# Performance work log

Hardware: AMD Instinct MI355X
Metric: run time of the kernel (lower is better)

## Reference

```python
import jax, jax.numpy as jnp
import numpy as np

B, S, H, L, NL = 64, 512, 768, 8, 10  # batch, seq, hidden, seps-per-sample ('longest'), num_labels

def setup_inputs() -> dict:
    key = jax.random.key(0)
    ks = jax.random.split(key, 16)
    sc = 0.05
    inp = {
        'electra_output': jax.random.normal(ks[0], (B, S, H), jnp.float32),
        # [SEP] locations: exactly L per sample -> mode count == L
        'sep_bx': jnp.repeat(jnp.arange(B, dtype=jnp.int64), L),
        'sep_by': jax.random.randint(ks[1], (B * L,), 1, S, dtype=jnp.int64),
        'w_ih_f': jax.random.normal(ks[2], (4 * H, H), jnp.float32) * sc,
        'w_hh_f': jax.random.normal(ks[3], (4 * H, H), jnp.float32) * sc,
        'b_ih_f': jax.random.normal(ks[4], (4 * H,), jnp.float32) * sc,
        'b_hh_f': jax.random.normal(ks[5], (4 * H,), jnp.float32) * sc,
        'w_ih_b': jax.random.normal(ks[6], (4 * H, H), jnp.float32) * sc,
        'w_hh_b': jax.random.normal(ks[7], (4 * H, H), jnp.float32) * sc,
        'b_ih_b': jax.random.normal(ks[8], (4 * H,), jnp.float32) * sc,
        'b_hh_b': jax.random.normal(ks[9], (4 * H,), jnp.float32) * sc,
        'fc1_w': jax.random.normal(ks[10], (NL, 5 * H), jnp.float32) * sc,
        'fc1_b': jax.random.normal(ks[11], (NL,), jnp.float32) * sc,
        'fc2_w': jax.random.normal(ks[12], (NL, 2 * H), jnp.float32) * sc,
        'fc2_b': jax.random.normal(ks[13], (NL,), jnp.float32) * sc,
    }
    return inp

def _lstm_dir(x, w_ih, w_hh, b_ih, b_hh):
    # x: [B, T, H] -> hs: [B, T, H]. PyTorch gate order: i, f, g, o.
    b, t, h = x.shape
    xg = jnp.einsum('bth,gh->btg', x, w_ih) + b_ih + b_hh  # [B,T,4H]
    def step(carry, xt):
        hprev, cprev = carry
        g = xt + hprev @ w_hh.T
        i, f, gg, o = jnp.split(g, 4, axis=-1)
        c = jax.nn.sigmoid(f) * cprev + jax.nn.sigmoid(i) * jnp.tanh(gg)
        hn = jax.nn.sigmoid(o) * jnp.tanh(c)
        return (hn, c), hn
    h0 = jnp.zeros((b, h), x.dtype)
    _, hs = jax.lax.scan(step, (h0, h0), jnp.swapaxes(xg, 0, 1))
    return jnp.swapaxes(hs, 0, 1)

def _forward(electra_output, sep_bx, sep_by, w_ih_f, w_hh_f, b_ih_f, b_hh_f,
             w_ih_b, w_hh_b, b_ih_b, b_hh_b, fc1_w, fc1_b, fc2_w, fc2_b):
    cls = electra_output[:, 0, :]  # [B,H]
    # Vectorized replacement of the per-token python loop: position of each
    # sep within its sample = index - first index of that sample's group.
    n = sep_bx.shape[0]
    ar = jnp.arange(n)
    starts = jax.ops.segment_min(ar, sep_bx, num_segments=B)
    pos = ar - starts[sep_bx]
    gathered = electra_output[sep_bx, sep_by]  # [N,H]
    sep_emb = jnp.zeros((B, L, H), electra_output.dtype).at[sep_bx, pos].add(gathered)
    # BiLSTM
    h_fwd = _lstm_dir(sep_emb, w_ih_f, w_hh_f, b_ih_f, b_hh_f)
    h_bwd = _lstm_dir(sep_emb[:, ::-1, :], w_ih_b, w_hh_b, b_ih_b, b_hh_b)[:, ::-1, :]
    lstm_out = jnp.concatenate([h_fwd, h_bwd], axis=-1)  # [B,L,2H]
    sep_first = lstm_out[:, 0, :]
    sep_last = lstm_out[:, -1, :]
    x = jax.nn.gelu(jnp.concatenate([cls, sep_first, sep_last], axis=1), approximate=False)
    output = x @ fc1_w.T + fc1_b
    first_output = sep_first @ fc2_w.T + fc2_b
    last_output = sep_last @ fc2_w.T + fc2_b
    return (output, first_output, last_output)

def reference(electra_output, sep_bx, sep_by, w_ih_f, w_hh_f, b_ih_f, b_hh_f,
              w_ih_b, w_hh_b, b_ih_b, b_hh_b, fc1_w, fc1_b, fc2_w, fc2_b):
    return _forward(electra_output, sep_bx, sep_by, w_ih_f, w_hh_f, b_ih_f, b_hh_f,
                    w_ih_b, w_hh_b, b_ih_b, b_hh_b, fc1_w, fc1_b, fc2_w, fc2_b)
```

## Files before the change

kernel.cpp:

```cpp
#include <hip/hip_runtime.h>
#include <math.h>

#define HID 768
#define NB 64
#define NL 8
#define SEQ 512
#define G4 3072

__device__ __forceinline__ float sigmoid_(float x) { return 1.0f / (1.0f + expf(-x)); }
__device__ __forceinline__ float gelu_(float x) { return 0.5f * x * (1.0f + erff(x * 0.70710678118654752440f)); }

__global__ void decode_idx_kernel(const void* __restrict__ sep_by, int n, int* __restrict__ out) {
    const int* p32 = (const int*)sep_by;
    const bool is64 = (p32[1] == 0) && (p32[3] == 0) && (p32[5] == 0) && (p32[7] == 0);
    int i = blockIdx.x * blockDim.x + threadIdx.x;
    if (i < n) {
        out[i] = is64 ? (int)((const long long*)sep_by)[i] : p32[i];
    }
}

__global__ __launch_bounds__(512) void xg_gemm_kernel(
    const float* __restrict__ electra, const int* __restrict__ idx,
    const float* __restrict__ w_ih_f, const float* __restrict__ w_ih_b,
    const float* __restrict__ b_ih_f, const float* __restrict__ b_hh_f,
    const float* __restrict__ b_ih_b, const float* __restrict__ b_hh_b,
    float* __restrict__ xg_f, float* __restrict__ xg_b)
{
    const int ng = blockIdx.x;
    const int mt = blockIdx.y;
    const int dir = blockIdx.z;
    const float* Wih = dir ? w_ih_b : w_ih_f;
    const float* BI  = dir ? b_ih_b : b_ih_f;
    const float* BH  = dir ? b_hh_b : b_hh_f;
    float* XG = dir ? xg_b : xg_f;

    const int tid = threadIdx.x;
    const int wave = tid >> 6, lane = tid & 63;
    const int n0 = __builtin_amdgcn_readfirstlane((ng * 8 + wave) * 8);

    const int m = mt * 64 + lane;
    const int b = m >> 3, t = m & 7;
    const int tt = dir ? (7 - t) : t;
    const int row = idx[b * 8 + tt];
    const float4* ap = (const float4*)(electra + ((size_t)b * SEQ + row) * HID);

    const float4* w0 = (const float4*)(Wih + (size_t)(n0 + 0) * HID);
    const float4* w1 = (const float4*)(Wih + (size_t)(n0 + 1) * HID);
    const float4* w2 = (const float4*)(Wih + (size_t)(n0 + 2) * HID);
    const float4* w3 = (const float4*)(Wih + (size_t)(n0 + 3) * HID);
    const float4* w4 = (const float4*)(Wih + (size_t)(n0 + 4) * HID);
    const float4* w5 = (const float4*)(Wih + (size_t)(n0 + 5) * HID);
    const float4* w6 = (const float4*)(Wih + (size_t)(n0 + 6) * HID);
    const float4* w7 = (const float4*)(Wih + (size_t)(n0 + 7) * HID);

    float a0 = 0.f, a1 = 0.f, a2 = 0.f, a3 = 0.f;
    float a4 = 0.f, a5 = 0.f, a6 = 0.f, a7 = 0.f;
#pragma unroll 2
    for (int kt = 0; kt < HID / 4; ++kt) {
        const float4 a = ap[kt];
        const float4 q0 = w0[kt];
        a0 = fmaf(a.x, q0.x, fmaf(a.y, q0.y, fmaf(a.z, q0.z, fmaf(a.w, q0.w, a0))));
        const float4 q1 = w1[kt];
        a1 = fmaf(a.x, q1.x, fmaf(a.y, q1.y, fmaf(a.z, q1.z, fmaf(a.w, q1.w, a1))));
        const float4 q2 = w2[kt];
        a2 = fmaf(a.x, q2.x, fmaf(a.y, q2.y, fmaf(a.z, q2.z, fmaf(a.w, q2.w, a2))));
        const float4 q3 = w3[kt];
        a3 = fmaf(a.x, q3.x, fmaf(a.y, q3.y, fmaf(a.z, q3.z, fmaf(a.w, q3.w, a3))));
        const float4 q4 = w4[kt];
        a4 = fmaf(a.x, q4.x, fmaf(a.y, q4.y, fmaf(a.z, q4.z, fmaf(a.w, q4.w, a4))));
        const float4 q5 = w5[kt];
        a5 = fmaf(a.x, q5.x, fmaf(a.y, q5.y, fmaf(a.z, q5.z, fmaf(a.w, q5.w, a5))));
        const float4 q6 = w6[kt];
        a6 = fmaf(a.x, q6.x, fmaf(a.y, q6.y, fmaf(a.z, q6.z, fmaf(a.w, q6.w, a6))));
        const float4 q7 = w7[kt];
        a7 = fmaf(a.x, q7.x, fmaf(a.y, q7.y, fmaf(a.z, q7.z, fmaf(a.w, q7.w, a7))));
    }

    float* outp = XG + (size_t)n0 * 512 + m;
    outp[0 * 512] = a0 + BI[n0 + 0] + BH[n0 + 0];
    outp[1 * 512] = a1 + BI[n0 + 1] + BH[n0 + 1];
    outp[2 * 512] = a2 + BI[n0 + 2] + BH[n0 + 2];
    outp[3 * 512] = a3 + BI[n0 + 3] + BH[n0 + 3];
    outp[4 * 512] = a4 + BI[n0 + 4] + BH[n0 + 4];
    outp[5 * 512] = a5 + BI[n0 + 5] + BH[n0 + 5];
    outp[6 * 512] = a6 + BI[n0 + 6] + BH[n0 + 6];
    outp[7 * 512] = a7 + BI[n0 + 7] + BH[n0 + 7];
}

__global__ __launch_bounds__(384) void lstm_step_kernel(
    const float* __restrict__ whh_f, const float* __restrict__ whh_b,
    const float* __restrict__ xg_f, const float* __restrict__ xg_b,
    const float* __restrict__ hcur, float* __restrict__ hnext,
    float* __restrict__ c_state, float* __restrict__ HF, float* __restrict__ HL,
    int s)
{
    const int bid = blockIdx.x;
    const int dir = bid >> 8;
    const int rem = bid & 255;
    const int tid = threadIdx.x;
    const int wave = tid >> 6;
    const int lane = tid & 63;
    const int jslot = wave >> 1;
    const int kh = wave & 1;
    const int j = rem * 3 + jslot;

    const float* WHH = dir ? whh_b : whh_f;
    const int jrow = __builtin_amdgcn_readfirstlane(j);
    const int kbase = __builtin_amdgcn_readfirstlane(kh * 384);
    const float4* wi = (const float4*)(WHH + (size_t)(0 * HID + jrow) * HID + kbase);
    const float4* wf = (const float4*)(WHH + (size_t)(1 * HID + jrow) * HID + kbase);
    const float4* wg = (const float4*)(WHH + (size_t)(2 * HID + jrow) * HID + kbase);
    const float4* wo = (const float4*)(WHH + (size_t)(3 * HID + jrow) * HID + kbase);
    const float* hp = hcur + ((size_t)dir * HID + kbase) * 64 + lane;

    float fi0 = 0.f, ff0 = 0.f, fg0 = 0.f, fo0 = 0.f;
    float fi1 = 0.f, ff1 = 0.f, fg1 = 0.f, fo1 = 0.f;
    if (s > 0) {
#pragma unroll 4
        for (int kt = 0; kt < 96; ++kt) {
            const float4 vi = wi[kt];
            const float4 vf = wf[kt];
            const float4 vg = wg[kt];
            const float4 vo = wo[kt];
            const float h0 = hp[(size_t)(kt * 4 + 0) * 64];
            const float h1 = hp[(size_t)(kt * 4 + 1) * 64];
            const float h2 = hp[(size_t)(kt * 4 + 2) * 64];
            const float h3 = hp[(size_t)(kt * 4 + 3) * 64];
            fi0 = fmaf(vi.x, h0, fmaf(vi.y, h1, fi0));
            fi1 = fmaf(vi.z, h2, fmaf(vi.w, h3, fi1));
            ff0 = fmaf(vf.x, h0, fmaf(vf.y, h1, ff0));
            ff1 = fmaf(vf.z, h2, fmaf(vf.w, h3, ff1));
            fg0 = fmaf(vg.x, h0, fmaf(vg.y, h1, fg0));
            fg1 = fmaf(vg.z, h2, fmaf(vg.w, h3, fg1));
            fo0 = fmaf(vo.x, h0, fmaf(vo.y, h1, fo0));
            fo1 = fmaf(vo.z, h2, fmaf(vo.w, h3, fo1));
        }
    }
    float fi = fi0 + fi1, ff = ff0 + ff1, fg = fg0 + fg1, fo = fo0 + fo1;

    __shared__ float red[2][3][4][64];
    red[kh][jslot][0][lane] = fi;
    red[kh][jslot][1][lane] = ff;
    red[kh][jslot][2][lane] = fg;
    red[kh][jslot][3][lane] = fo;
    __syncthreads();

    if (kh == 0) {
        fi += red[1][jslot][0][lane];
        ff += red[1][jslot][1][lane];
        fg += red[1][jslot][2][lane];
        fo += red[1][jslot][3][lane];

        const float* xgp = (dir ? xg_b : xg_f) + (size_t)j * 512 + lane * 8 + s;
        const float gi = sigmoid_(fi + xgp[0 * HID * 512]);
        const float gf = sigmoid_(ff + xgp[1 * HID * 512]);
        const float gg = tanhf (fg + xgp[2 * HID * 512]);
        const float go = sigmoid_(fo + xgp[3 * HID * 512]);

        const size_t slot = ((size_t)dir * HID + j) * 64 + lane;
        float c = (s == 0) ? 0.0f : c_state[slot];
        c = gf * c + gi * gg;
        c_state[slot] = c;
        const float hn = go * tanhf(c);
        hnext[slot] = hn;
        if (s == 0) HF[slot] = hn;
        if (s == 7) HL[slot] = hn;
    }
}

__device__ __forceinline__ void reduce10_(float* p, float* red, int tid,
                                          float* dst, const float* __restrict__ bias) {
#pragma unroll
    for (int o = 0; o < 10; ++o) {
        float v = p[o];
#pragma unroll
        for (int off = 32; off > 0; off >>= 1) v += __shfl_down(v, off);
        if ((tid & 63) == 0) red[o * 4 + (tid >> 6)] = v;
    }
    __syncthreads();
    if (tid < 10) dst[tid] = red[tid * 4 + 0] + red[tid * 4 + 1] + red[tid * 4 + 2] + red[tid * 4 + 3] + bias[tid];
    __syncthreads();
}

__global__ __launch_bounds__(256) void head_kernel(
    const float* __restrict__ electra, const float* __restrict__ HF,
    const float* __restrict__ HL,
    const float* __restrict__ fc1_w, const float* __restrict__ fc1_b,
    const float* __restrict__ fc2_w, const float* __restrict__ fc2_b,
    float* __restrict__ out)
{
    const int b = blockIdx.x;
    const int tid = threadIdx.x;
    __shared__ float xs[5 * HID];
    __shared__ float sf[2 * HID];
    __shared__ float sl[2 * HID];
    __shared__ float red[40];

    for (int k = tid; k < HID; k += 256) {
        xs[k] = gelu_(electra[(size_t)b * SEQ * HID + k]);
        const float v1 = HF[(size_t)k * 64 + b];
        const float v2 = HL[((size_t)HID + k) * 64 + b];
        const float v3 = HL[(size_t)k * 64 + b];
        const float v4 = HF[((size_t)HID + k) * 64 + b];
        sf[k] = v1;        xs[HID + k]     = gelu_(v1);
        sf[HID + k] = v2;  xs[2 * HID + k] = gelu_(v2);
        sl[k] = v3;        xs[3 * HID + k] = gelu_(v3);
        sl[HID + k] = v4;  xs[4 * HID + k] = gelu_(v4);
    }
    __syncthreads();

    {
        float p[10];
#pragma unroll
        for (int o = 0; o < 10; ++o) p[o] = 0.f;
        for (int k = tid; k < 5 * HID; k += 256) {
            const float xv = xs[k];
#pragma unroll
            for (int o = 0; o < 10; ++o) p[o] = fmaf(xv, fc1_w[o * (5 * HID) + k], p[o]);
        }
        reduce10_(p, red, tid, out + b * 10, fc1_b);
    }
    {
        float p[10];
#pragma unroll
        for (int o = 0; o < 10; ++o) p[o] = 0.f;
        for (int k = tid; k < 2 * HID; k += 256) {
            const float v = sf[k];
#pragma unroll
            for (int o = 0; o < 10; ++o) p[o] = fmaf(v, fc2_w[o * (2 * HID) + k], p[o]);
        }
        reduce10_(p, red, tid, out + 640 + b * 10, fc2_b);
    }
    {
        float p[10];
#pragma unroll
        for (int o = 0; o < 10; ++o) p[o] = 0.f;
        for (int k = tid; k < 2 * HID; k += 256) {
            const float v = sl[k];
#pragma unroll
            for (int o = 0; o < 10; ++o) p[o] = fmaf(v, fc2_w[o * (2 * HID) + k], p[o]);
        }
        reduce10_(p, red, tid, out + 1280 + b * 10, fc2_b);
    }
}

extern "C" void kernel_launch(void* const* d_in, const int* in_sizes, int n_in,
                              void* d_out, int out_size, void* d_ws, size_t ws_size,
                              hipStream_t stream) {
    const float* electra = (const float*)d_in[0];
    const void*  sep_by  = d_in[2];
    const float* w_ih_f  = (const float*)d_in[3];
    const float* w_hh_f  = (const float*)d_in[4];
    const float* b_ih_f  = (const float*)d_in[5];
    const float* b_hh_f  = (const float*)d_in[6];
    const float* w_ih_b  = (const float*)d_in[7];
    const float* w_hh_b  = (const float*)d_in[8];
    const float* b_ih_b  = (const float*)d_in[9];
    const float* b_hh_b  = (const float*)d_in[10];
    const float* fc1_w   = (const float*)d_in[11];
    const float* fc1_b   = (const float*)d_in[12];
    const float* fc2_w   = (const float*)d_in[13];
    const float* fc2_b   = (const float*)d_in[14];
    float* out = (float*)d_out;

    char* ws = (char*)d_ws;
    int*   idx     = (int*)(ws);
    float* xg_f    = (float*)(ws + 4096);
    float* xg_b    = (float*)(ws + 4096 + 6291456);
    char*  p2      = ws + 4096 + 2 * 6291456;
    float* hT      = (float*)(p2);
    float* c_state = (float*)(p2 + 786432);
    float* HF      = (float*)(p2 + 786432 + 393216);
    float* HL      = (float*)(p2 + 786432 + 2 * 393216);

    decode_idx_kernel<<<1, 512, 0, stream>>>(sep_by, NB * NL, idx);

    xg_gemm_kernel<<<dim3(48, 8, 2), 512, 0, stream>>>(
        electra, idx, w_ih_f, w_ih_b, b_ih_f, b_hh_f, b_ih_b, b_hh_b, xg_f, xg_b);

    const int PAR = 2 * HID * 64;
    for (int s = 0; s < 8; ++s) {
        const float* hcur = hT + (s & 1) * PAR;
        float* hnext = hT + ((s + 1) & 1) * PAR;
        lstm_step_kernel<<<512, 384, 0, stream>>>(
            w_hh_f, w_hh_b, xg_f, xg_b, hcur, hnext, c_state, HF, HL, s);
    }

    head_kernel<<<64, 256, 0, stream>>>(electra, HF, HL,
                                        fc1_w, fc1_b, fc2_w, fc2_b, out);
}
```

Baseline: 542.5 us.

## Tile input-projection GEMM via transposed operands and stage W_hh rows in LDS

Replaces the per-lane dot-product input projection with a shared-memory-tiled 128x128 register-blocked GEMM. The gathered activations and W_ih are first transposed into k-major buffers by two new kernels so that tiles can be read with coalesced loads. The LSTM step kernel now stages its 12 W_hh rows in LDS and reads the hidden state as float4 through a new interleaved h layout. This targets redundant global weight reads and poor reuse, at the cost of extra transpose passes and workspace traffic.

```diff
diff --git a/kernel.cpp b/kernel.cpp
--- a/kernel.cpp
+++ b/kernel.cpp
@@ -6,6 +6,7 @@
 #define NL 8
 #define SEQ 512
 #define G4 3072
+#define MTOT 512
 
 __device__ __forceinline__ float sigmoid_(float x) { return 1.0f / (1.0f + expf(-x)); }
 __device__ __forceinline__ float gelu_(float x) { return 0.5f * x * (1.0f + erff(x * 0.70710678118654752440f)); }
@@ -19,150 +20,218 @@
     }
 }
 
-__global__ __launch_bounds__(512) void xg_gemm_kernel(
+__global__ __launch_bounds__(256) void gatherT_kernel(
     const float* __restrict__ electra, const int* __restrict__ idx,
+    float* __restrict__ GT)
+{
+    const int kt = blockIdx.x;
+    const int mt = blockIdx.y;
+    const int dir = blockIdx.z;
+    __shared__ float T[64][65];
+    const int t = threadIdx.x;
+    const int k0 = kt * 64, m0 = mt * 64;
+#pragma unroll
+    for (int i = 0; i < 4; ++i) {
+        const int f4i = i * 256 + t;
+        const int ml = f4i >> 4;
+        const int k16 = f4i & 15;
+        const int m = m0 + ml;
+        const int b = m >> 3, ts0 = m & 7;
+        const int ts = dir ? (7 - ts0) : ts0;
+        const int row = idx[b * 8 + ts];
+        const float4 v = *(const float4*)(electra + ((size_t)b * SEQ + row) * HID + k0 + k16 * 4);
+        T[ml][k16 * 4 + 0] = v.x; T[ml][k16 * 4 + 1] = v.y;
+        T[ml][k16 * 4 + 2] = v.z; T[ml][k16 * 4 + 3] = v.w;
+    }
+    __syncthreads();
+#pragma unroll
+    for (int i = 0; i < 4; ++i) {
+        const int f4i = i * 256 + t;
+        const int kl = f4i >> 4;
+        const int m16 = f4i & 15;
+        float4 v;
+        v.x = T[m16 * 4 + 0][kl]; v.y = T[m16 * 4 + 1][kl];
+        v.z = T[m16 * 4 + 2][kl]; v.w = T[m16 * 4 + 3][kl];
+        *(float4*)(GT + ((size_t)dir * HID + k0 + kl) * MTOT + m0 + m16 * 4) = v;
+    }
+}
+
+__global__ __launch_bounds__(256) void transposeW_kernel(
     const float* __restrict__ w_ih_f, const float* __restrict__ w_ih_b,
+    float* __restrict__ WT)
+{
+    const int kt = blockIdx.x;
+    const int nt = blockIdx.y;
+    const int dir = blockIdx.z;
+    const float* W = dir ? w_ih_b : w_ih_f;
+    __shared__ float T[64][65];
+    const int t = threadIdx.x;
+    const int k0 = kt * 64, n0 = nt * 64;
+#pragma unroll
+    for (int i = 0; i < 4; ++i) {
+        const int f4i = i * 256 + t;
+        const int nl = f4i >> 4;
+        const int k16 = f4i & 15;
+        const float4 v = *(const float4*)(W + (size_t)(n0 + nl) * HID + k0 + k16 * 4);
+        T[nl][k16 * 4 + 0] = v.x; T[nl][k16 * 4 + 1] = v.y;
+        T[nl][k16 * 4 + 2] = v.z; T[nl][k16 * 4 + 3] = v.w;
+    }
+    __syncthreads();
+#pragma unroll
+    for (int i = 0; i < 4; ++i) {
+        const int f4i = i * 256 + t;
+        const int kl = f4i >> 4;
+        const int n16 = f4i & 15;
+        float4 v;
+        v.x = T[n16 * 4 + 0][kl]; v.y = T[n16 * 4 + 1][kl];
+        v.z = T[n16 * 4 + 2][kl]; v.w = T[n16 * 4 + 3][kl];
+        *(float4*)(WT + ((size_t)dir * HID + k0 + kl) * G4 + n0 + n16 * 4) = v;
+    }
+}
+
+__global__ __launch_bounds__(256) void xg_gemm_kernel(
+    const float* __restrict__ GT, const float* __restrict__ WT,
     const float* __restrict__ b_ih_f, const float* __restrict__ b_hh_f,
     const float* __restrict__ b_ih_b, const float* __restrict__ b_hh_b,
-    float* __restrict__ xg_f, float* __restrict__ xg_b)
-{
-    const int ng = blockIdx.x;
+    float* __restrict__ xg)
+{
+    const int nt = blockIdx.x;
     const int mt = blockIdx.y;
     const int dir = blockIdx.z;
-    const float* Wih = dir ? w_ih_b : w_ih_f;
-    const float* BI  = dir ? b_ih_b : b_ih_f;
-    const float* BH  = dir ? b_hh_b : b_hh_f;
-    float* XG = dir ? xg_b : xg_f;
-
-    const int tid = threadIdx.x;
-    const int wave = tid >> 6, lane = tid & 63;
-    const int n0 = __builtin_amdgcn_readfirstlane((ng * 8 + wave) * 8);
-
-    const int m = mt * 64 + lane;
-    const int b = m >> 3, t = m & 7;
-    const int tt = dir ? (7 - t) : t;
-    const int row = idx[b * 8 + tt];
-    const float4* ap = (const float4*)(electra + ((size_t)b * SEQ + row) * HID);
-
-    const float4* w0 = (const float4*)(Wih + (size_t)(n0 + 0) * HID);
-    const float4* w1 = (const float4*)(Wih + (size_t)(n0 + 1) * HID);
-    const float4* w2 = (const float4*)(Wih + (size_t)(n0 + 2) * HID);
-    const float4* w3 = (const float4*)(Wih + (size_t)(n0 + 3) * HID);
-    const float4* w4 = (const float4*)(Wih + (size_t)(n0 + 4) * HID);
-    const float4* w5 = (const float4*)(Wih + (size_t)(n0 + 5) * HID);
-    const float4* w6 = (const float4*)(Wih + (size_t)(n0 + 6) * HID);
-    const float4* w7 = (const float4*)(Wih + (size_t)(n0 + 7) * HID);
-
-    float a0 = 0.f, a1 = 0.f, a2 = 0.f, a3 = 0.f;
-    float a4 = 0.f, a5 = 0.f, a6 = 0.f, a7 = 0.f;
-#pragma unroll 2
-    for (int kt = 0; kt < HID / 4; ++kt) {
-        const float4 a = ap[kt];
-        const float4 q0 = w0[kt];
-        a0 = fmaf(a.x, q0.x, fmaf(a.y, q0.y, fmaf(a.z, q0.z, fmaf(a.w, q0.w, a0))));
-        const float4 q1 = w1[kt];
-        a1 = fmaf(a.x, q1.x, fmaf(a.y, q1.y, fmaf(a.z, q1.z, fmaf(a.w, q1.w, a1))));
-        const float4 q2 = w2[kt];
-        a2 = fmaf(a.x, q2.x, fmaf(a.y, q2.y, fmaf(a.z, q2.z, fmaf(a.w, q2.w, a2))));
-        const float4 q3 = w3[kt];
-        a3 = fmaf(a.x, q3.x, fmaf(a.y, q3.y, fmaf(a.z, q3.z, fmaf(a.w, q3.w, a3))));
-        const float4 q4 = w4[kt];
-        a4 = fmaf(a.x, q4.x, fmaf(a.y, q4.y, fmaf(a.z, q4.z, fmaf(a.w, q4.w, a4))));
-        const float4 q5 = w5[kt];
-        a5 = fmaf(a.x, q5.x, fmaf(a.y, q5.y, fmaf(a.z, q5.z, fmaf(a.w, q5.w, a5))));
-        const float4 q6 = w6[kt];
-        a6 = fmaf(a.x, q6.x, fmaf(a.y, q6.y, fmaf(a.z, q6.z, fmaf(a.w, q6.w, a6))));
-        const float4 q7 = w7[kt];
-        a7 = fmaf(a.x, q7.x, fmaf(a.y, q7.y, fmaf(a.z, q7.z, fmaf(a.w, q7.w, a7))));
-    }
-
-    float* outp = XG + (size_t)n0 * 512 + m;
-    outp[0 * 512] = a0 + BI[n0 + 0] + BH[n0 + 0];
-    outp[1 * 512] = a1 + BI[n0 + 1] + BH[n0 + 1];
-    outp[2 * 512] = a2 + BI[n0 + 2] + BH[n0 + 2];
-    outp[3 * 512] = a3 + BI[n0 + 3] + BH[n0 + 3];
-    outp[4 * 512] = a4 + BI[n0 + 4] + BH[n0 + 4];
-    outp[5 * 512] = a5 + BI[n0 + 5] + BH[n0 + 5];
-    outp[6 * 512] = a6 + BI[n0 + 6] + BH[n0 + 6];
-    outp[7 * 512] = a7 + BI[n0 + 7] + BH[n0 + 7];
-}
-
-__global__ __launch_bounds__(384) void lstm_step_kernel(
+    const float* BI = dir ? b_ih_b : b_ih_f;
+    const float* BH = dir ? b_hh_b : b_hh_f;
+    const float* gt = GT + (size_t)dir * HID * MTOT;
+    const float* wt = WT + (size_t)dir * HID * G4;
+    const int n0 = nt * 128, m0 = mt * 128;
+
+    __shared__ float As[16][128];
+    __shared__ float Ws[16][128];
+
+    const int t = threadIdx.x;
+    const int tx = t & 15, ty = t >> 4;
+    const int k1 = t >> 5;
+    const int k2 = 8 + (t >> 5);
+    const int m4 = t & 31;
+
+    float4 ra0, ra1, rw0, rw1;
+    ra0 = *(const float4*)(gt + (size_t)k1 * MTOT + m0 + m4 * 4);
+    ra1 = *(const float4*)(gt + (size_t)k2 * MTOT + m0 + m4 * 4);
+    rw0 = *(const float4*)(wt + (size_t)k1 * G4 + n0 + m4 * 4);
+    rw1 = *(const float4*)(wt + (size_t)k2 * G4 + n0 + m4 * 4);
+
+    float acc[8][8] = {};
+    for (int c = 0; c < 48; ++c) {
+        *(float4*)&As[k1][m4 * 4] = ra0;
+        *(float4*)&As[k2][m4 * 4] = ra1;
+        *(float4*)&Ws[k1][m4 * 4] = rw0;
+        *(float4*)&Ws[k2][m4 * 4] = rw1;
+        __syncthreads();
+        if (c < 47) {
+            const int kb = (c + 1) * 16;
+            ra0 = *(const float4*)(gt + (size_t)(kb + k1) * MTOT + m0 + m4 * 4);
+            ra1 = *(const float4*)(gt + (size_t)(kb + k2) * MTOT + m0 + m4 * 4);
+            rw0 = *(const float4*)(wt + (size_t)(kb + k1) * G4 + n0 + m4 * 4);
+            rw1 = *(const float4*)(wt + (size_t)(kb + k2) * G4 + n0 + m4 * 4);
+        }
+#pragma unroll
+        for (int k = 0; k < 16; ++k) {
+            float a[8], bb[8];
+            *(float4*)&a[0]  = *(const float4*)&As[k][ty * 8];
+            *(float4*)&a[4]  = *(const float4*)&As[k][ty * 8 + 4];
+            *(float4*)&bb[0] = *(const float4*)&Ws[k][tx * 8];
+            *(float4*)&bb[4] = *(const float4*)&Ws[k][tx * 8 + 4];
+#pragma unroll
+            for (int i = 0; i < 8; ++i)
+#pragma unroll
+                for (int j2 = 0; j2 < 8; ++j2)
+                    acc[i][j2] = fmaf(a[i], bb[j2], acc[i][j2]);
+        }
+        __syncthreads();
+    }
+
+    float* xgd = xg + (size_t)dir * G4 * MTOT;
+#pragma unroll
+    for (int j2 = 0; j2 < 8; ++j2) {
+        const int n = n0 + tx * 8 + j2;
+        const float bias = BI[n] + BH[n];
+        float4 o0, o1;
+        o0.x = acc[0][j2] + bias; o0.y = acc[1][j2] + bias;
+        o0.z = acc[2][j2] + bias; o0.w = acc[3][j2] + bias;
+        o1.x = acc[4][j2] + bias; o1.y = acc[5][j2] + bias;
+        o1.z = acc[6][j2] + bias; o1.w = acc[7][j2] + bias;
+        *(float4*)(xgd + (size_t)n * MTOT + m0 + ty * 8)     = o0;
+        *(float4*)(xgd + (size_t)n * MTOT + m0 + ty * 8 + 4) = o1;
+    }
+}
+
+__global__ __launch_bounds__(256) void lstm_step_kernel(
     const float* __restrict__ whh_f, const float* __restrict__ whh_b,
-    const float* __restrict__ xg_f, const float* __restrict__ xg_b,
-    const float* __restrict__ hcur, float* __restrict__ hnext,
+    const float* __restrict__ xg,
+    const float* __restrict__ hcur,
+    float* __restrict__ hnext,
     float* __restrict__ c_state, float* __restrict__ HF, float* __restrict__ HL,
     int s)
 {
-    const int bid = blockIdx.x;
-    const int dir = bid >> 8;
-    const int rem = bid & 255;
-    const int tid = threadIdx.x;
-    const int wave = tid >> 6;
-    const int lane = tid & 63;
-    const int jslot = wave >> 1;
-    const int kh = wave & 1;
-    const int j = rem * 3 + jslot;
-
+    const int jg = blockIdx.x;
+    const int dir = blockIdx.y;
     const float* WHH = dir ? whh_b : whh_f;
-    const int jrow = __builtin_amdgcn_readfirstlane(j);
-    const int kbase = __builtin_amdgcn_readfirstlane(kh * 384);
-    const float4* wi = (const float4*)(WHH + (size_t)(0 * HID + jrow) * HID + kbase);
-    const float4* wf = (const float4*)(WHH + (size_t)(1 * HID + jrow) * HID + kbase);
-    const float4* wg = (const float4*)(WHH + (size_t)(2 * HID + jrow) * HID + kbase);
-    const float4* wo = (const float4*)(WHH + (size_t)(3 * HID + jrow) * HID + kbase);
-    const float* hp = hcur + ((size_t)dir * HID + kbase) * 64 + lane;
-
-    float fi0 = 0.f, ff0 = 0.f, fg0 = 0.f, fo0 = 0.f;
-    float fi1 = 0.f, ff1 = 0.f, fg1 = 0.f, fo1 = 0.f;
+    const int t = threadIdx.x;
+
+    __shared__ float Wl[12][768];
+    __shared__ float red[12][64];
+
+#pragma unroll
+    for (int i = 0; i < 9; ++i) {
+        const int f4i = i * 256 + t;
+        const int r = f4i / 192;
+        const int k4 = f4i % 192;
+        const int jl = r >> 2, g = r & 3;
+        const int grow = g * HID + jg * 3 + jl;
+        *(float4*)&Wl[r][k4 * 4] = *(const float4*)(WHH + (size_t)grow * HID + k4 * 4);
+    }
+    __syncthreads();
+
+    const int wave = t >> 6, lane = t & 63;
+    const int r0 = wave * 3;
+    const float4* hp = (const float4*)hcur + (size_t)dir * 192 * 64 + lane;
+    float acc0 = 0.f, acc1 = 0.f, acc2 = 0.f;
     if (s > 0) {
 #pragma unroll 4
-        for (int kt = 0; kt < 96; ++kt) {
-            const float4 vi = wi[kt];
-            const float4 vf = wf[kt];
-            const float4 vg = wg[kt];
-            const float4 vo = wo[kt];
-            const float h0 = hp[(size_t)(kt * 4 + 0) * 64];
-            const float h1 = hp[(size_t)(kt * 4 + 1) * 64];
-            const float h2 = hp[(size_t)(kt * 4 + 2) * 64];
-            const float h3 = hp[(size_t)(kt * 4 + 3) * 64];
-            fi0 = fmaf(vi.x, h0, fmaf(vi.y, h1, fi0));
-            fi1 = fmaf(vi.z, h2, fmaf(vi.w, h3, fi1));
-            ff0 = fmaf(vf.x, h0, fmaf(vf.y, h1, ff0));
-            ff1 = fmaf(vf.z, h2, fmaf(vf.w, h3, ff1));
-            fg0 = fmaf(vg.x, h0, fmaf(vg.y, h1, fg0));
-            fg1 = fmaf(vg.z, h2, fmaf(vg.w, h3, fg1));
-            fo0 = fmaf(vo.x, h0, fmaf(vo.y, h1, fo0));
-            fo1 = fmaf(vo.z, h2, fmaf(vo.w, h3, fo1));
-        }
-    }
-    float fi = fi0 + fi1, ff = ff0 + ff1, fg = fg0 + fg1, fo = fo0 + fo1;
-
-    __shared__ float red[2][3][4][64];
-    red[kh][jslot][0][lane] = fi;
-    red[kh][jslot][1][lane] = ff;
-    red[kh][jslot][2][lane] = fg;
-    red[kh][jslot][3][lane] = fo;
-    __syncthreads();
-
-    if (kh == 0) {
-        fi += red[1][jslot][0][lane];
-        ff += red[1][jslot][1][lane];
-        fg += red[1][jslot][2][lane];
-        fo += red[1][jslot][3][lane];
-
-        const float* xgp = (dir ? xg_b : xg_f) + (size_t)j * 512 + lane * 8 + s;
-        const float gi = sigmoid_(fi + xgp[0 * HID * 512]);
-        const float gf = sigmoid_(ff + xgp[1 * HID * 512]);
-        const float gg = tanhf (fg + xgp[2 * HID * 512]);
-        const float go = sigmoid_(fo + xgp[3 * HID * 512]);
-
-        const size_t slot = ((size_t)dir * HID + j) * 64 + lane;
+        for (int k4 = 0; k4 < 192; ++k4) {
+            const float4 h = hp[(size_t)k4 * 64];
+            const float4 w0 = *(const float4*)&Wl[r0 + 0][k4 * 4];
+            const float4 w1 = *(const float4*)&Wl[r0 + 1][k4 * 4];
+            const float4 w2 = *(const float4*)&Wl[r0 + 2][k4 * 4];
+            acc0 = fmaf(w0.x, h.x, fmaf(w0.y, h.y, fmaf(w0.z, h.z, fmaf(w0.w, h.w, acc0))));
+            acc1 = fmaf(w1.x, h.x, fmaf(w1.y, h.y, fmaf(w1.z, h.z, fmaf(w1.w, h.w, acc1))));
+            acc2 = fmaf(w2.x, h.x, fmaf(w2.y, h.y, fmaf(w2.z, h.z, fmaf(w2.w, h.w, acc2))));
+        }
+    }
+    red[r0 + 0][lane] = acc0;
+    red[r0 + 1][lane] = acc1;
+    red[r0 + 2][lane] = acc2;
+    __syncthreads();
+
+    if (t < 192) {
+        const int jl = t >> 6;
+        const int b = t & 63;
+        const int j = jg * 3 + jl;
+        const float fi = red[jl * 4 + 0][b];
+        const float ff = red[jl * 4 + 1][b];
+        const float fg = red[jl * 4 + 2][b];
+        const float fo = red[jl * 4 + 3][b];
+        const float* xgp = xg + (size_t)dir * G4 * MTOT + (size_t)j * MTOT + b * 8 + s;
+        const float gi = sigmoid_(fi + xgp[0]);
+        const float gf = sigmoid_(ff + xgp[(size_t)1 * HID * MTOT]);
+        const float gg = tanhf (fg + xgp[(size_t)2 * HID * MTOT]);
+        const float go = sigmoid_(fo + xgp[(size_t)3 * HID * MTOT]);
+
+        const size_t slot = ((size_t)dir * HID + j) * 64 + b;
         float c = (s == 0) ? 0.0f : c_state[slot];
         c = gf * c + gi * gg;
         c_state[slot] = c;
         const float hn = go * tanhf(c);
-        hnext[slot] = hn;
+        hnext[(((size_t)dir * 192 + (j >> 2)) * 64 + b) * 4 + (j & 3)] = hn;
         if (s == 0) HF[slot] = hn;
         if (s == 7) HL[slot] = hn;
     }
@@ -265,25 +334,28 @@
 
     char* ws = (char*)d_ws;
     int*   idx     = (int*)(ws);
-    float* xg_f    = (float*)(ws + 4096);
-    float* xg_b    = (float*)(ws + 4096 + 6291456);
-    char*  p2      = ws + 4096 + 2 * 6291456;
-    float* hT      = (float*)(p2);
-    float* c_state = (float*)(p2 + 786432);
-    float* HF      = (float*)(p2 + 786432 + 393216);
-    float* HL      = (float*)(p2 + 786432 + 2 * 393216);
+    float* GT      = (float*)(ws + 4096);
+    float* WT      = (float*)(ws + 3149824);
+    float* XG      = (float*)(ws + 22024192);
+    float* hT      = (float*)(ws + 34607104);
+    float* c_state = (float*)(ws + 35393536);
+    float* HF      = (float*)(ws + 35786752);
+    float* HL      = (float*)(ws + 36179968);
 
     decode_idx_kernel<<<1, 512, 0, stream>>>(sep_by, NB * NL, idx);
 
-    xg_gemm_kernel<<<dim3(48, 8, 2), 512, 0, stream>>>(
-        electra, idx, w_ih_f, w_ih_b, b_ih_f, b_hh_f, b_ih_b, b_hh_b, xg_f, xg_b);
+    gatherT_kernel<<<dim3(12, 8, 2), 256, 0, stream>>>(electra, idx, GT);
+    transposeW_kernel<<<dim3(12, 48, 2), 256, 0, stream>>>(w_ih_f, w_ih_b, WT);
+
+    xg_gemm_kernel<<<dim3(24, 4, 2), 256, 0, stream>>>(
+        GT, WT, b_ih_f, b_hh_f, b_ih_b, b_hh_b, XG);
 
     const int PAR = 2 * HID * 64;
     for (int s = 0; s < 8; ++s) {
         const float* hcur = hT + (s & 1) * PAR;
         float* hnext = hT + ((s + 1) & 1) * PAR;
-        lstm_step_kernel<<<512, 384, 0, stream>>>(
-            w_hh_f, w_hh_b, xg_f, xg_b, hcur, hnext, c_state, HF, HL, s);
+        lstm_step_kernel<<<dim3(256, 2), 256, 0, stream>>>(
+            w_hh_f, w_hh_b, XG, hcur, hnext, c_state, HF, HL, s);
     }
 
     head_kernel<<<64, 256, 0, stream>>>(electra, HF, HL,
```

Result: faster. 448.0 us (-17.4%).
